# Performance work log

Measured on AMD Instinct MI355X. Metric: run time of the kernel, lower is better.

## Reference

```python
import jax, jax.numpy as jnp
import numpy as np

N = 100000      # nodes
E = 1600000     # edges
F_IN = 256      # input features
H = 128         # hidden_dim
C = 40          # num_classes
L = 4           # num_layers
STEP = 0.1


def setup_inputs() -> dict:
    key = jax.random.key(0)
    ks = jax.random.split(key, 8)
    s = 0.05
    return {
        "x": jax.random.normal(ks[0], (N, F_IN), jnp.float32),
        "edge_index": jax.random.randint(ks[1], (2, E), 0, N),
        "enc_W": jax.random.normal(ks[2], (H, F_IN), jnp.float32) * s,
        "enc_b": jnp.zeros((H,), jnp.float32),
        "W_raw": jax.random.normal(ks[3], (L, H, H + 2), jnp.float32) * s,
        "W_b": jnp.zeros((L, H), jnp.float32),
        "ext_w": jax.random.normal(ks[4], (L, H), jnp.float32),
        "beta": jax.random.normal(ks[5], (L,), jnp.float32),
        "dec_W": jax.random.normal(ks[6], (C, H), jnp.float32) * s,
        "dec_b": jnp.zeros((C,), jnp.float32),
    }


def _pairwise_weight(Wr):
    # Wr: (H, H+2) raw weight -> symmetric effective weight (H, H)
    W0 = jnp.triu(Wr[:, :-2], 1)
    W0 = W0 + W0.T
    diag = Wr[:, -2] * jnp.sum(jnp.abs(W0), axis=1) + Wr[:, -1]
    return W0 + jnp.diag(diag)


def reference(x, edge_index, enc_W, enc_b, W_raw, W_b, ext_w, beta, dec_W, dec_b):
    row, col = edge_index[0], edge_index[1]
    n = x.shape[0]
    # degree over source nodes (edge_index[0]), recomputed identically each layer
    deg = jnp.zeros((n,), x.dtype).at[row].add(jnp.float32(1.0))
    deg_inv = jnp.where(deg > 0, jnp.where(deg > 0, deg, 1.0) ** -0.5, 0.0)
    # message = deg_inv[row]*deg_inv[col] * x_i (x_i = features of target col),
    # scatter-added at target col  ==>  per-node coefficient times node feature
    coef = jnp.zeros((n,), x.dtype).at[col].add(deg_inv[row] * deg_inv[col])

    h = x @ enc_W.T + enc_b
    h0 = h
    for l in range(W_raw.shape[0]):
        W_eff = _pairwise_weight(W_raw[l])        # symmetric (H,H)
        out_p = h @ W_eff.T + W_b[l]              # pairwise linear transform
        agg = coef[:, None] * out_p               # gather+normalize+scatter-add
        out = agg - (h * ext_w[l][None, :] + beta[l] * h0)
        h = h + STEP * jax.nn.relu(out)
    return h @ dec_W.T + dec_b
```

## Files before the change

### kernel.cpp

```cpp
#include <hip/hip_runtime.h>

typedef unsigned int u32;
typedef unsigned short u16;
typedef __bf16 bf16x8 __attribute__((ext_vector_type(8)));
typedef float f32x16 __attribute__((ext_vector_type(16)));
typedef u32 u32x4 __attribute__((ext_vector_type(4)));

#define HDIM 128
#define FIN  256
#define NCLS 40
#define NL   4
#define BN   16384
#define NSL  32

__device__ __forceinline__ u16 f2b(float f){
  union { __bf16 h; u16 s; } u; u.h = (__bf16)f; return u.s;
}
__device__ __forceinline__ u32 pk(float a, float b){
  union { __bf16 h[2]; u32 w; } u; u.h[0] = (__bf16)a; u.h[1] = (__bf16)b; return u.w;
}
__device__ __forceinline__ float ubf(u32 hbits){
  union { u32 w; float f; } u; u.w = hbits << 16; return u.f;
}
__device__ __forceinline__ float dinv(float d){ return d > 0.f ? rsqrtf(d) : 0.f; }

__device__ __forceinline__ int fragIdx128(int row, int k){
  return (((((row >> 5) * 8 + (k >> 4)) * 2 + ((k >> 3) & 1)) * 32 + (row & 31)) * 8) + (k & 7);
}

__global__ void prep_kernel(const float* __restrict__ encW, const float* __restrict__ Wraw,
                            const float* __restrict__ decW,
                            u16* __restrict__ encF, u16* __restrict__ weffF, u16* __restrict__ decB){
  int b = blockIdx.x, t = threadIdx.x;
  if(b < 512){
    int i = b * 64 + t;
    int row = i >> 8, k = i & 255;
    int chunk = k >> 7, kk = k & 127;
    encF[chunk * 16384 + fragIdx128(row, kk)] = f2b(encW[i]);
  } else if(b < 1024){
    int idx = b - 512;
    int l = idx >> 7, i = idx & 127;
    const float* Wr = Wraw + (size_t)l * HDIM * (HDIM + 2);
    float w0a, w0b, s = 0.f;
    { int j = t;
      float v = (i < j) ? Wr[i*(HDIM+2)+j] : ((j < i) ? Wr[j*(HDIM+2)+i] : 0.f);
      w0a = v; s += fabsf(v); }
    { int j = t + 64;
      float v = (i < j) ? Wr[i*(HDIM+2)+j] : ((j < i) ? Wr[j*(HDIM+2)+i] : 0.f);
      w0b = v; s += fabsf(v); }
    #pragma unroll
    for(int d = 1; d < 64; d <<= 1) s += __shfl_xor(s, d, 64);
    float diag = Wr[i*(HDIM+2)+HDIM] * s + Wr[i*(HDIM+2)+HDIM+1];
    u16* o = weffF + (size_t)l * 16384;
    o[fragIdx128(i, t)]      = f2b((t == i)      ? diag : w0a);
    o[fragIdx128(i, t + 64)] = f2b((t + 64 == i) ? diag : w0b);
  } else {
    int idx = b - 1024;
    int i = idx * 64 + t;
    int c = i >> 7, k = i & 127;
    decB[i] = (c < NCLS) ? f2b(decW[c * HDIM + k]) : (u16)0;
  }
}


template<int WEIGHTED>
__global__ void __launch_bounds__(256, 2)
hist_kernel(const int* __restrict__ idx, const int* __restrict__ src,
            const float* __restrict__ dv, float* __restrict__ partial,
            int E, int Nn, int NB, int chunk)
{
  __shared__ float buck[BN];
  const int tid = threadIdx.x;
  const int g = blockIdx.x % NB;
  const int s = blockIdx.x / NB;
  const int lo = g << 14;

  for(int i = tid; i < BN; i += 256) buck[i] = 0.f;
  __syncthreads();

  long e0 = (long)s * chunk;
  long e1 = (long)E < e0 + chunk ? (long)E : e0 + chunk;
  if(e0 < e1){
    long ng = (e1 - e0) >> 2;
    for(long gi = tid; gi < ng; gi += 256){
      long e = e0 + gi * 4;
      int4 c = *(const int4*)(idx + e);
      int4 r;
      if(WEIGHTED) r = *(const int4*)(src + e);
      int k;
      k = c.x - lo; if((u32)k < (u32)BN) atomicAdd(&buck[k], WEIGHTED ? dv[r.x] : 1.f);
      k = c.y - lo; if((u32)k < (u32)BN) atomicAdd(&buck[k], WEIGHTED ? dv[r.y] : 1.f);
      k = c.z - lo; if((u32)k < (u32)BN) atomicAdd(&buck[k], WEIGHTED ? dv[r.z] : 1.f);
      k = c.w - lo; if((u32)k < (u32)BN) atomicAdd(&buck[k], WEIGHTED ? dv[r.w] : 1.f);
    }
    long et = e0 + ng * 4;
    if(et + tid < e1){
      long e = et + tid;
      int k = idx[e] - lo;
      if((u32)k < (u32)BN) atomicAdd(&buck[k], WEIGHTED ? dv[src[e]] : 1.f);
    }
  }
  __syncthreads();

  float* dst = partial + (size_t)s * ((size_t)NB << 14) + lo;
  int hi = Nn - lo < BN ? Nn - lo : BN;
  for(int i = tid; i < hi; i += 256) dst[i] = buck[i];
}

template<int MODE>
__global__ void reduce_kernel(const float* __restrict__ partial, const float* __restrict__ dvin,
                              float* __restrict__ outv, int Nn, int NB, int S)
{
  int i = blockIdx.x * 256 + threadIdx.x;
  if(i >= Nn) return;
  const size_t NnPad = (size_t)NB << 14;
  float t = 0.f;
  for(int s = 0; s < S; s++) t += partial[(size_t)s * NnPad + i];
  outv[i] = MODE ? dvin[i] * t : (t > 0.f ? rsqrtf(t) : 0.f);
}


__global__ void deg_kernel(const int* __restrict__ ei, float* __restrict__ deg, int E){
  long e = ((long)blockIdx.x * 256 + threadIdx.x) * 8;
  if(e + 7 < E){
    int4 v0 = *(const int4*)(ei + e);
    int4 v1 = *(const int4*)(ei + e + 4);
    atomicAdd(&deg[v0.x], 1.0f); atomicAdd(&deg[v0.y], 1.0f);
    atomicAdd(&deg[v0.z], 1.0f); atomicAdd(&deg[v0.w], 1.0f);
    atomicAdd(&deg[v1.x], 1.0f); atomicAdd(&deg[v1.y], 1.0f);
    atomicAdd(&deg[v1.z], 1.0f); atomicAdd(&deg[v1.w], 1.0f);
  } else {
    for(; e < E; e++) atomicAdd(&deg[ei[e]], 1.0f);
  }
}

__global__ void coef_kernel(const int* __restrict__ ei, const float* __restrict__ deg,
                            float* __restrict__ coef, int E){
  long e = ((long)blockIdx.x * 256 + threadIdx.x) * 8;
  if(e + 7 < E){
    int4 r0 = *(const int4*)(ei + e);
    int4 r1 = *(const int4*)(ei + e + 4);
    int4 c0 = *(const int4*)(ei + E + e);
    int4 c1 = *(const int4*)(ei + E + e + 4);
    atomicAdd(&coef[c0.x], dinv(deg[r0.x]) * dinv(deg[c0.x]));
    atomicAdd(&coef[c0.y], dinv(deg[r0.y]) * dinv(deg[c0.y]));
    atomicAdd(&coef[c0.z], dinv(deg[r0.z]) * dinv(deg[c0.z]));
    atomicAdd(&coef[c0.w], dinv(deg[r0.w]) * dinv(deg[c0.w]));
    atomicAdd(&coef[c1.x], dinv(deg[r1.x]) * dinv(deg[c1.x]));
    atomicAdd(&coef[c1.y], dinv(deg[r1.y]) * dinv(deg[c1.y]));
    atomicAdd(&coef[c1.z], dinv(deg[r1.z]) * dinv(deg[c1.z]));
    atomicAdd(&coef[c1.w], dinv(deg[r1.w]) * dinv(deg[c1.w]));
  } else {
    for(; e < E; e++){
      int r = ei[e], c = ei[E + e];
      atomicAdd(&coef[c], dinv(deg[r]) * dinv(deg[c]));
    }
  }
}

__device__ __forceinline__ bf16x8 buildBp(u32 P0, u32 P1, u32 P2, u32 P3, int hi){
  u32 S0 = hi ? P0 : P2;
  u32 S1 = hi ? P1 : P3;
  u32 R0 = __shfl_xor(S0, 32, 64);
  u32 R1 = __shfl_xor(S1, 32, 64);
  union { u32 w[4]; bf16x8 b; } u;
  u.w[0] = hi ? R0 : P0;
  u.w[1] = hi ? R1 : P1;
  u.w[2] = hi ? P2 : R0;
  u.w[3] = hi ? P3 : R1;
  return u.b;
}

__device__ __forceinline__ void stage32k(u16* __restrict__ lds, const u16* __restrict__ src, int tid){
  const u32x4* s = (const u32x4*)src;
  u32x4* d = (u32x4*)lds;
  #pragma unroll
  for(int i = 0; i < 8; i++) d[tid + i * 256] = s[tid + i * 256];
}

__global__ void __launch_bounds__(256, 1)
enc_kernel(const float* __restrict__ x, const float* __restrict__ enc_b,
           const u16* __restrict__ encF, u32* __restrict__ h0F, int Nn)
{
  __shared__ u16 lw[16384];
  __shared__ u16 xc[16384];

  const int tid  = threadIdx.x;
  const int lane = tid & 63;
  const int hi   = lane >> 5;
  const int ln   = lane & 31;
  const int nib  = (tid >> 6) * 32 + ln;
  const int blk  = blockIdx.x;

  f32x16 acc[4];
  #pragma unroll
  for(int nt = 0; nt < 4; nt++)
    #pragma unroll
    for(int i = 0; i < 16; i++) acc[nt][i] = 0.f;

  const int r0 = tid >> 5;
  const int c4 = (tid & 31) * 4;
  const int g  = c4 >> 3, j = c4 & 7;

  for(int chunk = 0; chunk < 2; chunk++){
    __syncthreads();
    stage32k(lw, encF + chunk * 16384, tid);
    #pragma unroll
    for(int i = 0; i < 16; i++){
      int r = i * 8 + r0;
      int gn = blk * 128 + r; if(gn >= Nn) gn = Nn - 1;
      float4 v = *(const float4*)(x + (size_t)gn * FIN + chunk * 128 + c4);
      u32* d = (u32*)(xc + g * 1024 + ((r ^ (g & 7)) << 3) + j);
      d[0] = pk(v.x, v.y);
      d[1] = pk(v.z, v.w);
    }
    __syncthreads();

    #pragma unroll
    for(int ksl = 0; ksl < 8; ksl++){
      #pragma unroll
      for(int nt = 0; nt < 4; nt++){
        const int gg = ksl * 2 + hi;
        const bf16x8 B = *(const bf16x8*)(xc + gg * 1024 + ((nib ^ (gg & 7)) << 3));
        const bf16x8 A = *(const bf16x8*)(lw + ((((nt * 8 + ksl) * 2 + hi) * 32 + ln) * 8));
        acc[nt] = __builtin_amdgcn_mfma_f32_32x32x16_bf16(A, B, acc[nt], 0, 0, 0);
      }
    }
  }

  u32* dst = h0F + (size_t)blk * 8192;
  #pragma unroll
  for(int nt = 0; nt < 4; nt++){
    #pragma unroll
    for(int q = 0; q < 4; q++){
      float4 eb = *(const float4*)(enc_b + nt * 32 + 8 * q + 4 * hi);
      acc[nt][4*q+0] += eb.x; acc[nt][4*q+1] += eb.y;
      acc[nt][4*q+2] += eb.z; acc[nt][4*q+3] += eb.w;
    }
    #pragma unroll
    for(int m = 0; m < 8; m++)
      dst[(nt * 8 + m) * 256 + tid] = pk(acc[nt][2*m], acc[nt][2*m+1]);
  }
}

__global__ void __launch_bounds__(256, 1)
lay_kernel(const float* __restrict__ W_b, const float* __restrict__ ext_w,
           const float* __restrict__ beta, const float* __restrict__ dec_b,
           const float* __restrict__ coef, const u32* __restrict__ h0F,
           const u16* __restrict__ weffF, const u16* __restrict__ decB,
           float* __restrict__ out, int Nn)
{
  __shared__ u16 lw[16384];
  __shared__ u32 h0s[32][256];

  const int tid  = threadIdx.x;
  const int lane = tid & 63;
  const int wv   = tid >> 6;
  const int hi   = lane >> 5;
  const int ln   = lane & 31;
  const int nib  = wv * 32 + ln;
  const int node = blockIdx.x * 128 + nib;
  const int nd   = node < Nn ? node : (Nn - 1);
  const float cf = coef[nd];

  u32 hp[32];
  const u32* src = h0F + (size_t)blockIdx.x * 8192;
  #pragma unroll
  for(int m = 0; m < 32; m++){
    u32 w = src[m * 256 + tid];
    hp[m] = w;
    h0s[m][tid] = w;
  }

  for(int l = 0; l < NL; l++){
    __syncthreads();
    stage32k(lw, weffF + l * 16384, tid);
    __syncthreads();

    const float bet = beta[l];
    u32 hn[16];

    #pragma unroll
    for(int P = 0; P < 2; P++){
      f32x16 a0, a1;
      #pragma unroll
      for(int i = 0; i < 16; i++){ a0[i] = 0.f; a1[i] = 0.f; }

      #pragma unroll
      for(int ks = 0; ks < 8; ks++){
        const int wbase = (ks >> 1) * 8 + 4 * (ks & 1);
        bf16x8 B = buildBp(hp[wbase+0], hp[wbase+1], hp[wbase+2], hp[wbase+3], hi);
        const bf16x8 A0 = *(const bf16x8*)(lw + (((((2*P+0) * 8 + ks) * 2 + hi) * 32 + ln) * 8));
        const bf16x8 A1 = *(const bf16x8*)(lw + (((((2*P+1) * 8 + ks) * 2 + hi) * 32 + ln) * 8));
        a0 = __builtin_amdgcn_mfma_f32_32x32x16_bf16(A0, B, a0, 0, 0, 0);
        a1 = __builtin_amdgcn_mfma_f32_32x32x16_bf16(A1, B, a1, 0, 0, 0);
      }

      #pragma unroll
      for(int t = 0; t < 2; t++){
        const int nt = 2*P + t;
        f32x16& a = t ? a1 : a0;
        #pragma unroll
        for(int q = 0; q < 4; q++){
          const int fb = nt * 32 + 8 * q + 4 * hi;
          float4 wb = *(const float4*)(W_b   + l * HDIM + fb);
          float4 ew = *(const float4*)(ext_w + l * HDIM + fb);
          #pragma unroll
          for(int r2 = 0; r2 < 4; r2++){
            const int r = 4 * q + r2;
            float wbv = (r2==0)?wb.x:(r2==1)?wb.y:(r2==2)?wb.z:wb.w;
            float ewv = (r2==0)?ew.x:(r2==1)?ew.y:(r2==2)?ew.z:ew.w;
            u32 w0 = h0s[nt * 8 + (r >> 1)][tid];
            u32 wc = hp[nt * 8 + (r >> 1)];
            float h0v = ubf((r & 1) ? (w0 >> 16) : (w0 & 0xffffu));
            float hv  = ubf((r & 1) ? (wc >> 16) : (wc & 0xffffu));
            float o = cf * (a[r] + wbv) - hv * ewv - bet * h0v;
            a[r] = hv + 0.1f * fmaxf(o, 0.f);
          }
        }
        #pragma unroll
        for(int m = 0; m < 8; m++){
          u32 w = pk(a[2*m], a[2*m+1]);
          if(P == 0) hn[nt * 8 + m] = w;
          else       hp[nt * 8 + m] = w;
        }
      }
    }
    #pragma unroll
    for(int m = 0; m < 16; m++) hp[m] = hn[m];
  }

  f32x16 d0, d1;
  #pragma unroll
  for(int i = 0; i < 16; i++){ d0[i] = 0.f; d1[i] = 0.f; }

  #pragma unroll
  for(int ks = 0; ks < 8; ks++){
    const int wbase = (ks >> 1) * 8 + 4 * (ks & 1);
    bf16x8 B = buildBp(hp[wbase+0], hp[wbase+1], hp[wbase+2], hp[wbase+3], hi);
    const bf16x8 A0 = *(const bf16x8*)(decB + (0 * 32 + ln) * HDIM + ks * 16 + hi * 8);
    const bf16x8 A1 = *(const bf16x8*)(decB + (1 * 32 + ln) * HDIM + ks * 16 + hi * 8);
    d0 = __builtin_amdgcn_mfma_f32_32x32x16_bf16(A0, B, d0, 0, 0, 0);
    d1 = __builtin_amdgcn_mfma_f32_32x32x16_bf16(A1, B, d1, 0, 0, 0);
  }

  if(node < Nn){
    #pragma unroll
    for(int nt = 0; nt < 2; nt++){
      const f32x16& d = nt ? d1 : d0;
      #pragma unroll
      for(int q = 0; q < 4; q++){
        if(nt == 0 || q == 0){
          const int c0 = nt * 32 + 8 * q + 4 * hi;
          float4 db = *(const float4*)(dec_b + c0);
          float4 v;
          v.x = d[4*q+0] + db.x;
          v.y = d[4*q+1] + db.y;
          v.z = d[4*q+2] + db.z;
          v.w = d[4*q+3] + db.w;
          *(float4*)(out + (size_t)node * NCLS + c0) = v;
        }
      }
    }
  }
}

extern "C" void kernel_launch(void* const* d_in, const int* in_sizes, int n_in,
                              void* d_out, int out_size, void* d_ws, size_t ws_size,
                              hipStream_t stream){
  (void)n_in; (void)out_size;
  const float* x     = (const float*)d_in[0];
  const int*   ei    = (const int*)  d_in[1];
  const float* encW  = (const float*)d_in[2];
  const float* enc_b = (const float*)d_in[3];
  const float* Wraw  = (const float*)d_in[4];
  const float* W_b   = (const float*)d_in[5];
  const float* ext_w = (const float*)d_in[6];
  const float* beta  = (const float*)d_in[7];
  const float* decW  = (const float*)d_in[8];
  const float* dec_b = (const float*)d_in[9];
  float* out = (float*)d_out;
  const int Nn = in_sizes[0] / FIN;
  const int E  = in_sizes[1] / 2;
  const int nBlk = (Nn + 127) / 128;
  const int NB   = (Nn + BN - 1) / BN;
  const int chunk = (((E + NSL - 1) / NSL) + 3) & ~3;

  char* ws = (char*)d_ws;
  size_t szN = ((size_t)Nn * 4 + 511) & ~(size_t)511;
  float* coef = (float*)(ws);
  float* dv   = (float*)(ws + szN);
  u16* encF   = (u16*)(ws + 2 * szN);
  u16* weffF  = (u16*)(ws + 2 * szN + 65536);
  u16* decB   = (u16*)(ws + 2 * szN + 65536 + 131072);
  u32* h0F    = (u32*)(ws + 2 * szN + 65536 + 131072 + 16384);
  float* partial = (float*)(ws + 2 * szN + 65536 + 131072 + 16384 + (size_t)nBlk * 32768);
  const size_t partialBytes = (size_t)NSL * ((size_t)NB << 14) * 4;
  const size_t need = 2 * szN + 65536 + 131072 + 16384 + (size_t)nBlk * 32768 + partialBytes;
  const bool fast = ws_size >= need;

  prep_kernel<<<1152, 64, 0, stream>>>(encW, Wraw, decW, encF, weffF, decB);
  const int ngrid = (Nn + 255) / 256;
  if(fast){
    hist_kernel<0><<<NB * NSL, 256, 0, stream>>>(ei, ei, dv, partial, E, Nn, NB, chunk);
    reduce_kernel<0><<<ngrid, 256, 0, stream>>>(partial, dv, dv, Nn, NB, NSL);
    hist_kernel<1><<<NB * NSL, 256, 0, stream>>>(ei + E, ei, dv, partial, E, Nn, NB, chunk);
    reduce_kernel<1><<<ngrid, 256, 0, stream>>>(partial, dv, coef, Nn, NB, NSL);
  } else {
    const int egrid = (int)((E / 8 + 255) / 256) + 1;
    hipMemsetAsync(ws, 0, 2 * szN, stream);
    deg_kernel <<<egrid, 256, 0, stream>>>(ei, dv, E);
    coef_kernel<<<egrid, 256, 0, stream>>>(ei, dv, coef, E);
  }
  enc_kernel <<<nBlk, 256, 0, stream>>>(x, enc_b, encF, h0F, Nn);
  lay_kernel <<<nBlk, 256, 0, stream>>>(W_b, ext_w, beta, dec_b, coef, h0F, weffF, decB, out, Nn);
}
```

Baseline: 195.1 us.

## Double-buffer per-half weight staging in LDS and allow two blocks per CU

Splits each layer's 32KB effective-weight staging into two 16KB halves held in a double buffer. The next half is prefetched from global memory into registers while the current half's MFMAs and epilogue run, then written to the other buffer before a single barrier. This hides the global-load latency that previously sat between two barriers. Launch bounds also change from 1 to 2 blocks per CU, which caps register usage and may cause spills given the large per-thread hp/hn/accumulator state.

```diff
diff --git a/kernel.cpp b/kernel.cpp
--- a/kernel.cpp
+++ b/kernel.cpp
@@ -243,14 +243,14 @@
   }
 }
 
-__global__ void __launch_bounds__(256, 1)
+__global__ void __launch_bounds__(256, 2)
 lay_kernel(const float* __restrict__ W_b, const float* __restrict__ ext_w,
            const float* __restrict__ beta, const float* __restrict__ dec_b,
            const float* __restrict__ coef, const u32* __restrict__ h0F,
            const u16* __restrict__ weffF, const u16* __restrict__ decB,
            float* __restrict__ out, int Nn)
 {
-  __shared__ u16 lw[16384];
+  __shared__ u16 lw[2][8192];
   __shared__ u32 h0s[32][256];
 
   const int tid  = threadIdx.x;
@@ -272,62 +272,81 @@
     h0s[m][tid] = w;
   }
 
-  for(int l = 0; l < NL; l++){
-    __syncthreads();
-    stage32k(lw, weffF + l * 16384, tid);
-    __syncthreads();
+  {
+    const u32x4* s = (const u32x4*)weffF;
+    u32x4* d = (u32x4*)lw[0];
+    #pragma unroll
+    for(int i = 0; i < 4; i++) d[tid + i * 256] = s[tid + i * 256];
+  }
+  __syncthreads();
+
+  u32 hn[16];
+  #pragma unroll
+  for(int p = 0; p < 2 * NL; p++){
+    const int l = p >> 1, P = p & 1, cur = p & 1;
+
+    u32x4 g[4];
+    if(p < 2 * NL - 1){
+      const u32x4* s2 = (const u32x4*)(weffF + (size_t)((p+1) >> 1) * 16384 + ((p+1) & 1) * 8192);
+      #pragma unroll
+      for(int i = 0; i < 4; i++) g[i] = s2[tid + i * 256];
+    }
 
     const float bet = beta[l];
-    u32 hn[16];
-
-    #pragma unroll
-    for(int P = 0; P < 2; P++){
-      f32x16 a0, a1;
-      #pragma unroll
-      for(int i = 0; i < 16; i++){ a0[i] = 0.f; a1[i] = 0.f; }
-
-      #pragma unroll
-      for(int ks = 0; ks < 8; ks++){
-        const int wbase = (ks >> 1) * 8 + 4 * (ks & 1);
-        bf16x8 B = buildBp(hp[wbase+0], hp[wbase+1], hp[wbase+2], hp[wbase+3], hi);
-        const bf16x8 A0 = *(const bf16x8*)(lw + (((((2*P+0) * 8 + ks) * 2 + hi) * 32 + ln) * 8));
-        const bf16x8 A1 = *(const bf16x8*)(lw + (((((2*P+1) * 8 + ks) * 2 + hi) * 32 + ln) * 8));
-        a0 = __builtin_amdgcn_mfma_f32_32x32x16_bf16(A0, B, a0, 0, 0, 0);
-        a1 = __builtin_amdgcn_mfma_f32_32x32x16_bf16(A1, B, a1, 0, 0, 0);
-      }
-
-      #pragma unroll
-      for(int t = 0; t < 2; t++){
-        const int nt = 2*P + t;
-        f32x16& a = t ? a1 : a0;
+    f32x16 a0, a1;
+    #pragma unroll
+    for(int i = 0; i < 16; i++){ a0[i] = 0.f; a1[i] = 0.f; }
+
+    #pragma unroll
+    for(int ks = 0; ks < 8; ks++){
+      const int wbase = (ks >> 1) * 8 + 4 * (ks & 1);
+      bf16x8 B = buildBp(hp[wbase+0], hp[wbase+1], hp[wbase+2], hp[wbase+3], hi);
+      const bf16x8 A0 = *(const bf16x8*)(lw[cur] + ((((0 * 8 + ks) * 2 + hi) * 32 + ln) * 8));
+      const bf16x8 A1 = *(const bf16x8*)(lw[cur] + ((((1 * 8 + ks) * 2 + hi) * 32 + ln) * 8));
+      a0 = __builtin_amdgcn_mfma_f32_32x32x16_bf16(A0, B, a0, 0, 0, 0);
+      a1 = __builtin_amdgcn_mfma_f32_32x32x16_bf16(A1, B, a1, 0, 0, 0);
+    }
+
+    #pragma unroll
+    for(int t = 0; t < 2; t++){
+      const int nt = 2 * P + t;
+      f32x16& a = t ? a1 : a0;
+      #pragma unroll
+      for(int q = 0; q < 4; q++){
+        const int fb = nt * 32 + 8 * q + 4 * hi;
+        float4 wb = *(const float4*)(W_b   + l * HDIM + fb);
+        float4 ew = *(const float4*)(ext_w + l * HDIM + fb);
         #pragma unroll
-        for(int q = 0; q < 4; q++){
-          const int fb = nt * 32 + 8 * q + 4 * hi;
-          float4 wb = *(const float4*)(W_b   + l * HDIM + fb);
-          float4 ew = *(const float4*)(ext_w + l * HDIM + fb);
-          #pragma unroll
-          for(int r2 = 0; r2 < 4; r2++){
-            const int r = 4 * q + r2;
-            float wbv = (r2==0)?wb.x:(r2==1)?wb.y:(r2==2)?wb.z:wb.w;
-            float ewv = (r2==0)?ew.x:(r2==1)?ew.y:(r2==2)?ew.z:ew.w;
-            u32 w0 = h0s[nt * 8 + (r >> 1)][tid];
-            u32 wc = hp[nt * 8 + (r >> 1)];
-            float h0v = ubf((r & 1) ? (w0 >> 16) : (w0 & 0xffffu));
-            float hv  = ubf((r & 1) ? (wc >> 16) : (wc & 0xffffu));
-            float o = cf * (a[r] + wbv) - hv * ewv - bet * h0v;
-            a[r] = hv + 0.1f * fmaxf(o, 0.f);
-          }
-        }
-        #pragma unroll
-        for(int m = 0; m < 8; m++){
-          u32 w = pk(a[2*m], a[2*m+1]);
-          if(P == 0) hn[nt * 8 + m] = w;
-          else       hp[nt * 8 + m] = w;
+        for(int r2 = 0; r2 < 4; r2++){
+          const int r = 4 * q + r2;
+          float wbv = (r2==0)?wb.x:(r2==1)?wb.y:(r2==2)?wb.z:wb.w;
+          float ewv = (r2==0)?ew.x:(r2==1)?ew.y:(r2==2)?ew.z:ew.w;
+          u32 w0 = h0s[nt * 8 + (r >> 1)][tid];
+          u32 wc = hp[nt * 8 + (r >> 1)];
+          float h0v = ubf((r & 1) ? (w0 >> 16) : (w0 & 0xffffu));
+          float hv  = ubf((r & 1) ? (wc >> 16) : (wc & 0xffffu));
+          float o = cf * (a[r] + wbv) - hv * ewv - bet * h0v;
+          a[r] = hv + 0.1f * fmaxf(o, 0.f);
         }
       }
-    }
-    #pragma unroll
-    for(int m = 0; m < 16; m++) hp[m] = hn[m];
+      #pragma unroll
+      for(int m = 0; m < 8; m++){
+        u32 w = pk(a[2*m], a[2*m+1]);
+        if(P == 0) hn[nt * 8 + m] = w;
+        else       hp[nt * 8 + m] = w;
+      }
+    }
+    if(P == 1){
+      #pragma unroll
+      for(int m = 0; m < 16; m++) hp[m] = hn[m];
+    }
+
+    if(p < 2 * NL - 1){
+      u32x4* d2 = (u32x4*)lw[cur ^ 1];
+      #pragma unroll
+      for(int i = 0; i < 4; i++) d2[tid + i * 256] = g[i];
+    }
+    __syncthreads();
   }
 
   f32x16 d0, d1;
```

Measured after the change: 208.7 us. 7.0% more time.
